# Performance work log

Measured on AMD Instinct MI355X. Metric: run time of the kernel, lower is better.

## Reference

```python
import jax, jax.numpy as jnp
import numpy as np

N_NODES = 100000
N_EDGES = 1600000
IN_DIM = 128
OUT_DIM = 128


def setup_inputs() -> dict:
    key = jax.random.key(0)
    k1, k2, k3, k4, k5 = jax.random.split(key, 5)
    h = jax.random.normal(k1, (N_NODES, IN_DIM), dtype=jnp.float32)
    # nn.Linear(in_dim, out_dim): W [out, in], b [out]
    W = jax.random.normal(k2, (OUT_DIM, IN_DIM), dtype=jnp.float32) * (1.0 / np.sqrt(IN_DIM))
    b = jax.random.normal(k3, (OUT_DIM,), dtype=jnp.float32) * 0.01
    edge_src = jax.random.randint(k4, (N_EDGES,), 0, N_NODES, dtype=jnp.int32)
    edge_dst = jax.random.randint(k5, (N_EDGES,), 0, N_NODES, dtype=jnp.int32)
    return {"h": h, "W": W, "b": b, "edge_src": edge_src, "edge_dst": edge_dst}


def reference(h, W, b, edge_src, edge_dst):
    n = h.shape[0]
    # in-degree of each node (edges point src -> dst), clamped to >= 1
    deg = jax.ops.segment_sum(jnp.ones_like(edge_dst, dtype=h.dtype), edge_dst, num_segments=n)
    norm = jnp.power(jnp.clip(deg, 1.0), -0.5)[:, None]  # [N, 1]
    hn = h * norm
    # copy_u + sum: gather source features, scatter-add to destinations (SpMM)
    agg = jax.ops.segment_sum(hn[edge_src], edge_dst, num_segments=n)  # [N, in_dim]
    out = (agg * norm) @ W.T + b
    return out
```

## Files before the change

kernel.cpp:

```cpp
#include <hip/hip_runtime.h>
#include <hip/hip_fp16.h>

#define DIM 128
#define TSH 8
#define TSZ 256
#define EBLK 4096

typedef _Float16 half8_t __attribute__((ext_vector_type(8)));
typedef float f32x4 __attribute__((ext_vector_type(4)));
typedef float f32x4v __attribute__((ext_vector_type(4)));


__global__ __launch_bounds__(1024) void hist_a(const int* __restrict__ dst,
                                               int* __restrict__ gh,
                                               int ne, int nblk, int nt,
                                               const float* __restrict__ W,
                                               _Float16* __restrict__ Wf) {
    __shared__ int h[512];
    int t = threadIdx.x;
    int blk = blockIdx.x;
    if (blk >= nblk) {
        int idx = (blk - nblk) * 1024 + t;
        int tile = idx >> 8;
        int kk = (idx >> 6) & 3;
        int lane = idx & 63;
        int nn = lane & 15, quad = lane >> 4;
        const float* wr = W + (tile * 16 + nn) * DIM + kk * 32 + quad * 8;
        _Float16* o = Wf + (size_t)idx * 8;
#pragma unroll
        for (int j = 0; j < 8; ++j) o[j] = (_Float16)wr[j];
        return;
    }
    if (t < 512) h[t] = 0;
    __syncthreads();
    int i0 = blk * EBLK + t;
#pragma unroll
    for (int u = 0; u < 4; ++u) {
        int i = i0 + u * 1024;
        if (i < ne) atomicAdd(&h[dst[i] >> TSH], 1);
    }
    __syncthreads();
    for (int k = t; k < nt; k += 1024) gh[k * nblk + blk] = h[k];
}

__global__ __launch_bounds__(256) void scan_a(int* __restrict__ g,
                                              int* __restrict__ bsum, int M) {
    __shared__ int wsum[4];
    int t = threadIdx.x;
    int base = blockIdx.x * 1024 + t * 4;
    int4 v;
    if (base + 3 < M) v = *(const int4*)(g + base);
    else {
        v.x = (base + 0 < M) ? g[base + 0] : 0;
        v.y = (base + 1 < M) ? g[base + 1] : 0;
        v.z = (base + 2 < M) ? g[base + 2] : 0;
        v.w = (base + 3 < M) ? g[base + 3] : 0;
    }
    int s3 = v.x + v.y + v.z + v.w;
    int lane = t & 63, wv = t >> 6;
    int x = s3;
#pragma unroll
    for (int off = 1; off < 64; off <<= 1) {
        int y = __shfl_up(x, off, 64);
        if (lane >= off) x += y;
    }
    if (lane == 63) wsum[wv] = x;
    __syncthreads();
    int woff = 0;
    for (int i = 0; i < wv; ++i) woff += wsum[i];
    int ex = woff + x - s3;
    int4 o;
    o.x = ex; o.y = ex + v.x; o.z = o.y + v.y; o.w = o.z + v.z;
    if (base + 3 < M) *(int4*)(g + base) = o;
    else {
        if (base + 0 < M) g[base + 0] = o.x;
        if (base + 1 < M) g[base + 1] = o.y;
        if (base + 2 < M) g[base + 2] = o.z;
        if (base + 3 < M) g[base + 3] = o.w;
    }
    if (t == 0) bsum[blockIdx.x] = wsum[0] + wsum[1] + wsum[2] + wsum[3];
}

__global__ __launch_bounds__(1024) void scatter_b(const int* __restrict__ src,
                                                  const int* __restrict__ dst,
                                                  const int* __restrict__ gh,
                                                  const int* __restrict__ bsum,
                                                  unsigned* __restrict__ tbuf,
                                                  int ne, int nblk, int M, int nt,
                                                  int nsc) {
    __shared__ int hD[512];
    __shared__ int ps[256];
    __shared__ int cur[512];
    __shared__ int gbl[256];
    __shared__ unsigned sval[EBLK];
    __shared__ unsigned short skey[EBLK];
    int t = threadIdx.x, blk = blockIdx.x;

    int bd = 0;
    if (t < 256) { bd = (t < nsc) ? bsum[t] : 0; ps[t] = bd; }
    __syncthreads();
    for (int off = 1; off < 256; off <<= 1) {
        int v = (t < 256 && t >= off) ? ps[t - off] : 0;
        __syncthreads();
        if (t < 256) ps[t] += v;
        __syncthreads();
    }
    if (t < 256) gbl[t] = ps[t] - bd;
    __syncthreads();

    int p0 = 0, c = 0;
    if (t < 512) {
        if (t < nt) {
            int idx = t * nblk + blk;
            p0 = gh[idx] + gbl[idx >> 10];
            int p1 = (idx + 1 < M) ? (gh[idx + 1] + gbl[(idx + 1) >> 10]) : ne;
            c = p1 - p0;
        }
        hD[t] = c;
    }
    __syncthreads();
    int h0 = 0, h1 = 0;
    if (t < 256) { h0 = hD[2 * t]; h1 = hD[2 * t + 1]; ps[t] = h0 + h1; }
    __syncthreads();
    for (int off = 1; off < 256; off <<= 1) {
        int v = (t < 256 && t >= off) ? ps[t - off] : 0;
        __syncthreads();
        if (t < 256) ps[t] += v;
        __syncthreads();
    }
    if (t < 256) {
        int ex0 = ps[t] - h0 - h1;
        cur[2 * t] = ex0;
        cur[2 * t + 1] = ex0 + h0;
    }
    __syncthreads();
    if (t < 512) hD[t] = p0 - cur[t];
    __syncthreads();

    int i0 = blk * EBLK + t;
#pragma unroll
    for (int u = 0; u < 4; ++u) {
        int i = i0 + u * 1024;
        if (i < ne) {
            int d = dst[i];
            int key = d >> TSH;
            int r = atomicAdd(&cur[key], 1);
            sval[r] = ((unsigned)src[i] << TSH) | (unsigned)(d & (TSZ - 1));
            skey[r] = (unsigned short)key;
        }
    }
    __syncthreads();
    int cnt = ne - blk * EBLK;
    if (cnt > EBLK) cnt = EBLK;
    for (int p = t; p < cnt; p += 1024)
        tbuf[hD[skey[p]] + p] = sval[p];
}

__global__ __launch_bounds__(1024) void tile_sort(const unsigned* __restrict__ tbuf,
                                                  const int* __restrict__ gh,
                                                  const int* __restrict__ bsum,
                                                  int* __restrict__ ebuf,
                                                  int* __restrict__ row_start,
                                                  const float* __restrict__ hsrc,
                                                  float2* __restrict__ hn,
                                                  int n, int ne, int nblk, int nt,
                                                  int nsc) {
    __shared__ int hist[TSZ];
    __shared__ int cur[TSZ];
    __shared__ int ps[256];
    __shared__ int gbl[256];
    __shared__ float scl[TSZ];
    int t = threadIdx.x;
    int tile = blockIdx.x;

    int bd = 0;
    if (t < 256) { bd = (t < nsc) ? bsum[t] : 0; ps[t] = bd; hist[t] = 0; }
    __syncthreads();
    for (int off = 1; off < 256; off <<= 1) {
        int v = (t < 256 && t >= off) ? ps[t - off] : 0;
        __syncthreads();
        if (t < 256) ps[t] += v;
        __syncthreads();
    }
    if (t < 256) gbl[t] = ps[t] - bd;
    __syncthreads();

    int i0 = tile * nblk;
    int ts = gh[i0] + gbl[i0 >> 10];
    int i1 = (tile + 1) * nblk;
    int te = (tile + 1 < nt) ? gh[i1] + gbl[i1 >> 10] : ne;

    for (int i = ts + t; i < te; i += 1024)
        atomicAdd(&hist[tbuf[i] & (TSZ - 1)], 1);
    __syncthreads();
    int d = 0;
    if (t < 256) { d = hist[t]; ps[t] = d; }
    __syncthreads();
    for (int off = 1; off < 256; off <<= 1) {
        int v = (t < 256 && t >= off) ? ps[t - off] : 0;
        __syncthreads();
        if (t < 256) ps[t] += v;
        __syncthreads();
    }
    if (t < 256) {
        int ex = ps[t] - d;
        cur[t] = ex;
        int node = tile * TSZ + t;
        if (node <= n) row_start[node] = ts + ex;
        scl[t] = rsqrtf((float)(d > 1 ? d : 1));
    }
    __syncthreads();
    for (int i = ts + t; i < te; i += 1024) {
        unsigned p = tbuf[i];
        int dl = (int)(p & (TSZ - 1));
        int r = atomicAdd(&cur[dl], 1);
        ebuf[ts + r] = (int)(p >> TSH);
    }
    int qbase = tile * 8192;
    for (int q = t; q < 8192; q += 1024) {
        int node = tile * TSZ + (q >> 5);
        if (node < n) {
            f32x4v v = __builtin_nontemporal_load((const f32x4v*)hsrc + qbase + q);
            float sc = scl[q >> 5];
            union { __half2 h2[2]; float2 f2; } u;
            u.h2[0] = __floats2half2_rn(v.x * sc, v.y * sc);
            u.h2[1] = __floats2half2_rn(v.z * sc, v.w * sc);
            hn[qbase + q] = u.f2;
        }
    }
}

__global__ __launch_bounds__(512) void gather_gemm(const float2* __restrict__ hn,
                                                   const int* __restrict__ ebuf,
                                                   const int* __restrict__ rs,
                                                   const _Float16* __restrict__ Wf,
                                                   const float* __restrict__ b,
                                                   float* __restrict__ out, int n) {
    __shared__ _Float16 xs[64 * 136];
    int tid = threadIdx.x;
    int g = tid >> 5, lane = tid & 31;

#pragma unroll
    for (int it = 0; it < 4; ++it) {
        int row = it * 16 + g;
        int node = blockIdx.x * 64 + row;
        union { __half2 h2[2]; float2 f2; } u;
        if (node < n) {
            int s0 = rs[node];
            int s1 = rs[node + 1];
            __half2 a0 = __floats2half2_rn(0.f, 0.f), a1 = a0;
            int i = s0;
            for (; i + 7 < s1; i += 8) {
                int e0 = ebuf[i], e1 = ebuf[i + 1], e2 = ebuf[i + 2], e3 = ebuf[i + 3];
                int e4 = ebuf[i + 4], e5 = ebuf[i + 5], e6 = ebuf[i + 6], e7 = ebuf[i + 7];
                float2 r0 = hn[(size_t)e0 * 32 + lane];
                float2 r1 = hn[(size_t)e1 * 32 + lane];
                float2 r2 = hn[(size_t)e2 * 32 + lane];
                float2 r3 = hn[(size_t)e3 * 32 + lane];
                float2 r4 = hn[(size_t)e4 * 32 + lane];
                float2 r5 = hn[(size_t)e5 * 32 + lane];
                float2 r6 = hn[(size_t)e6 * 32 + lane];
                float2 r7 = hn[(size_t)e7 * 32 + lane];
                const __half2* q0 = (const __half2*)&r0;
                const __half2* q1 = (const __half2*)&r1;
                const __half2* q2 = (const __half2*)&r2;
                const __half2* q3 = (const __half2*)&r3;
                const __half2* q4 = (const __half2*)&r4;
                const __half2* q5 = (const __half2*)&r5;
                const __half2* q6 = (const __half2*)&r6;
                const __half2* q7 = (const __half2*)&r7;
                a0 = __hadd2(a0, q0[0]); a1 = __hadd2(a1, q0[1]);
                a0 = __hadd2(a0, q1[0]); a1 = __hadd2(a1, q1[1]);
                a0 = __hadd2(a0, q2[0]); a1 = __hadd2(a1, q2[1]);
                a0 = __hadd2(a0, q3[0]); a1 = __hadd2(a1, q3[1]);
                a0 = __hadd2(a0, q4[0]); a1 = __hadd2(a1, q4[1]);
                a0 = __hadd2(a0, q5[0]); a1 = __hadd2(a1, q5[1]);
                a0 = __hadd2(a0, q6[0]); a1 = __hadd2(a1, q6[1]);
                a0 = __hadd2(a0, q7[0]); a1 = __hadd2(a1, q7[1]);
            }
            for (; i + 3 < s1; i += 4) {
                int e0 = ebuf[i], e1 = ebuf[i + 1], e2 = ebuf[i + 2], e3 = ebuf[i + 3];
                float2 r0 = hn[(size_t)e0 * 32 + lane];
                float2 r1 = hn[(size_t)e1 * 32 + lane];
                float2 r2 = hn[(size_t)e2 * 32 + lane];
                float2 r3 = hn[(size_t)e3 * 32 + lane];
                const __half2* q0 = (const __half2*)&r0;
                const __half2* q1 = (const __half2*)&r1;
                const __half2* q2 = (const __half2*)&r2;
                const __half2* q3 = (const __half2*)&r3;
                a0 = __hadd2(a0, q0[0]); a1 = __hadd2(a1, q0[1]);
                a0 = __hadd2(a0, q1[0]); a1 = __hadd2(a1, q1[1]);
                a0 = __hadd2(a0, q2[0]); a1 = __hadd2(a1, q2[1]);
                a0 = __hadd2(a0, q3[0]); a1 = __hadd2(a1, q3[1]);
            }
            for (; i < s1; ++i) {
                int e0 = ebuf[i];
                float2 r0 = hn[(size_t)e0 * 32 + lane];
                const __half2* q0 = (const __half2*)&r0;
                a0 = __hadd2(a0, q0[0]); a1 = __hadd2(a1, q0[1]);
            }
            int dn = s1 - s0;
            float nd = rsqrtf((float)(dn > 1 ? dn : 1));
            float2 f0 = __half22float2(a0), f1 = __half22float2(a1);
            u.h2[0] = __floats2half2_rn(f0.x * nd, f0.y * nd);
            u.h2[1] = __floats2half2_rn(f1.x * nd, f1.y * nd);
        } else {
            u.h2[0] = __floats2half2_rn(0.f, 0.f);
            u.h2[1] = u.h2[0];
        }
        *(float2*)(xs + row * 136 + lane * 4) = u.f2;
    }
    __syncthreads();

    int w = tid >> 6;
    int wl = tid & 63;
    int cn = wl & 15;
    int quad = wl >> 4;

    f32x4 acc[4] = {{0.f, 0.f, 0.f, 0.f}, {0.f, 0.f, 0.f, 0.f},
                    {0.f, 0.f, 0.f, 0.f}, {0.f, 0.f, 0.f, 0.f}};
#pragma unroll
    for (int kk = 0; kk < 4; ++kk) {
        half8_t bf = ((const half8_t*)Wf)[(w * 4 + kk) * 64 + wl];
#pragma unroll
        for (int rt = 0; rt < 4; ++rt) {
            half8_t af = *(const half8_t*)(xs + (rt * 16 + cn) * 136 + kk * 32 + quad * 8);
            acc[rt] = __builtin_amdgcn_mfma_f32_16x16x32_f16(af, bf, acc[rt], 0, 0, 0);
        }
    }
    float bj = b[w * 16 + cn];
    int node0 = blockIdx.x * 64;
#pragma unroll
    for (int rt = 0; rt < 4; ++rt) {
#pragma unroll
        for (int r = 0; r < 4; ++r) {
            int node = node0 + rt * 16 + quad * 4 + r;
            if (node < n)
                __builtin_nontemporal_store(acc[rt][r] + bj,
                                            &out[(size_t)node * DIM + w * 16 + cn]);
        }
    }
}

extern "C" void kernel_launch(void* const* d_in, const int* in_sizes, int n_in,
                              void* d_out, int out_size, void* d_ws, size_t ws_size,
                              hipStream_t stream) {
    const float* h = (const float*)d_in[0];
    const float* W = (const float*)d_in[1];
    const float* b = (const float*)d_in[2];
    const int* esrc = (const int*)d_in[3];
    const int* edst = (const int*)d_in[4];
    float* out = (float*)d_out;

    int n = in_sizes[0] / DIM;
    int ne = in_sizes[3];

    int nblk = (ne + EBLK - 1) / EBLK;
    int nt = (n + TSZ - 1) >> TSH;
    int M = nt * nblk;
    int nsc = (M + 1023) / 1024;

    float2* hn = (float2*)d_ws;
    _Float16* Wf = (_Float16*)(hn + (size_t)n * 32);
    int* row_start = (int*)(Wf + 16384);
    int* gh = row_start + (n + 1);
    int* gbsum = gh + M;
    unsigned* tbuf = (unsigned*)(gbsum + 256);
    int* ebuf = (int*)(tbuf + ne);

    hist_a<<<nblk + 2, 1024, 0, stream>>>(edst, gh, ne, nblk, nt, W, Wf);
    scan_a<<<nsc, 256, 0, stream>>>(gh, gbsum, M);
    scatter_b<<<nblk, 1024, 0, stream>>>(esrc, edst, gh, gbsum, tbuf, ne, nblk, M, nt, nsc);
    tile_sort<<<nt, 1024, 0, stream>>>(tbuf, gh, gbsum, ebuf, row_start, h, hn, n, ne, nblk, nt, nsc);
    gather_gemm<<<(n + 63) / 64, 512, 0, stream>>>(hn, ebuf, row_start, Wf, b, out, n);
}
```

Baseline: 216.4 us.

## Fuse per-tile edge sort with gather and GEMM, compute degrees via global atomics

Computes in-degree with global atomics in the histogram kernel and moves fp16 feature normalization into the scan kernel. The tile-sort kernel is merged with the gather+GEMM kernel, so each 256-node tile buckets its edges in LDS and aggregates and multiplies them directly. This removes the ebuf/row_start round trip and one launch. In exchange, the grid shrinks to about 391 large blocks with heavy LDS use, which lowers parallelism for the latency-bound gather. There is also a slow fallback path when a tile has more edges than fit in LDS.

```diff
diff --git a/kernel.cpp b/kernel.cpp
--- a/kernel.cpp
+++ b/kernel.cpp
@@ -5,27 +5,26 @@
 #define TSH 8
 #define TSZ 256
 #define EBLK 4096
+#define CAP 4608
 
 typedef _Float16 half8_t __attribute__((ext_vector_type(8)));
 typedef float f32x4 __attribute__((ext_vector_type(4)));
 typedef float f32x4v __attribute__((ext_vector_type(4)));
 
 
-__global__ __launch_bounds__(1024) void hist_a(const int* __restrict__ dst,
-                                               int* __restrict__ gh,
-                                               int ne, int nblk, int nt,
-                                               const float* __restrict__ W,
-                                               _Float16* __restrict__ Wf) {
+__global__ __launch_bounds__(1024) void k1_hist(const int* __restrict__ dst,
+                                                int* __restrict__ gh,
+                                                int* __restrict__ deg,
+                                                int ne, int neb, int nt,
+                                                const float* __restrict__ W,
+                                                _Float16* __restrict__ Wf) {
     __shared__ int h[512];
-    int t = threadIdx.x;
-    int blk = blockIdx.x;
-    if (blk >= nblk) {
-        int idx = (blk - nblk) * 1024 + t;
-        int tile = idx >> 8;
-        int kk = (idx >> 6) & 3;
-        int lane = idx & 63;
+    int t = threadIdx.x, blk = blockIdx.x;
+    if (blk >= neb) {
+        int idx = (blk - neb) * 1024 + t;
+        int ct = idx >> 8, kk = (idx >> 6) & 3, lane = idx & 63;
         int nn = lane & 15, quad = lane >> 4;
-        const float* wr = W + (tile * 16 + nn) * DIM + kk * 32 + quad * 8;
+        const float* wr = W + (ct * 16 + nn) * DIM + kk * 32 + quad * 8;
         _Float16* o = Wf + (size_t)idx * 8;
 #pragma unroll
         for (int j = 0; j < 8; ++j) o[j] = (_Float16)wr[j];
@@ -33,61 +32,69 @@
     }
     if (t < 512) h[t] = 0;
     __syncthreads();
-    int i0 = blk * EBLK + t;
-#pragma unroll
-    for (int u = 0; u < 4; ++u) {
-        int i = i0 + u * 1024;
-        if (i < ne) atomicAdd(&h[dst[i] >> TSH], 1);
-    }
-    __syncthreads();
-    for (int k = t; k < nt; k += 1024) gh[k * nblk + blk] = h[k];
-}
-
-__global__ __launch_bounds__(256) void scan_a(int* __restrict__ g,
-                                              int* __restrict__ bsum, int M) {
-    __shared__ int wsum[4];
-    int t = threadIdx.x;
-    int base = blockIdx.x * 1024 + t * 4;
-    int4 v;
-    if (base + 3 < M) v = *(const int4*)(g + base);
-    else {
-        v.x = (base + 0 < M) ? g[base + 0] : 0;
-        v.y = (base + 1 < M) ? g[base + 1] : 0;
-        v.z = (base + 2 < M) ? g[base + 2] : 0;
-        v.w = (base + 3 < M) ? g[base + 3] : 0;
-    }
-    int s3 = v.x + v.y + v.z + v.w;
-    int lane = t & 63, wv = t >> 6;
-    int x = s3;
-#pragma unroll
-    for (int off = 1; off < 64; off <<= 1) {
-        int y = __shfl_up(x, off, 64);
-        if (lane >= off) x += y;
-    }
-    if (lane == 63) wsum[wv] = x;
-    __syncthreads();
-    int woff = 0;
-    for (int i = 0; i < wv; ++i) woff += wsum[i];
-    int ex = woff + x - s3;
-    int4 o;
-    o.x = ex; o.y = ex + v.x; o.z = o.y + v.y; o.w = o.z + v.z;
-    if (base + 3 < M) *(int4*)(g + base) = o;
-    else {
-        if (base + 0 < M) g[base + 0] = o.x;
-        if (base + 1 < M) g[base + 1] = o.y;
-        if (base + 2 < M) g[base + 2] = o.z;
-        if (base + 3 < M) g[base + 3] = o.w;
-    }
-    if (t == 0) bsum[blockIdx.x] = wsum[0] + wsum[1] + wsum[2] + wsum[3];
-}
-
-__global__ __launch_bounds__(1024) void scatter_b(const int* __restrict__ src,
-                                                  const int* __restrict__ dst,
-                                                  const int* __restrict__ gh,
-                                                  const int* __restrict__ bsum,
-                                                  unsigned* __restrict__ tbuf,
-                                                  int ne, int nblk, int M, int nt,
-                                                  int nsc) {
+    int e0 = blk * EBLK;
+    int e1 = e0 + EBLK; if (e1 > ne) e1 = ne;
+    for (int i = e0 + t; i < e1; i += 1024) {
+        int d = dst[i];
+        atomicAdd(&h[d >> TSH], 1);
+        atomicAdd(&deg[d], 1);
+    }
+    __syncthreads();
+    for (int k = t; k < nt; k += 1024) gh[k * neb + blk] = h[k];
+}
+
+__global__ __launch_bounds__(1024) void k2_scan_hn(int* __restrict__ g,
+                                                   int* __restrict__ bsum,
+                                                   int M, int nsc,
+                                                   const int* __restrict__ deg,
+                                                   const float* __restrict__ hsrc,
+                                                   float2* __restrict__ hn,
+                                                   int n32) {
+    int t = threadIdx.x, blk = blockIdx.x;
+    if (blk < nsc) {
+        __shared__ int wsum[16];
+        int base = blk * 1024 + t;
+        int v = (base < M) ? g[base] : 0;
+        int lane = t & 63, wv = t >> 6;
+        int x = v;
+#pragma unroll
+        for (int off = 1; off < 64; off <<= 1) {
+            int y = __shfl_up(x, off, 64);
+            if (lane >= off) x += y;
+        }
+        if (lane == 63) wsum[wv] = x;
+        __syncthreads();
+        int woff = 0;
+        for (int i = 0; i < wv; ++i) woff += wsum[i];
+        if (base < M) g[base] = woff + x - v;
+        if (t == 0) {
+            int s = 0;
+#pragma unroll
+            for (int i = 0; i < 16; ++i) s += wsum[i];
+            bsum[blk] = s;
+        }
+        return;
+    }
+    int q = (blk - nsc) * 1024 + t;
+    if (q < n32) {
+        int node = q >> 5;
+        int dg = deg[node];
+        float sc = rsqrtf((float)(dg > 1 ? dg : 1));
+        f32x4v v = __builtin_nontemporal_load((const f32x4v*)hsrc + q);
+        union { __half2 h2[2]; float2 f2; } u;
+        u.h2[0] = __floats2half2_rn(v.x * sc, v.y * sc);
+        u.h2[1] = __floats2half2_rn(v.z * sc, v.w * sc);
+        hn[q] = u.f2;
+    }
+}
+
+__global__ __launch_bounds__(1024) void k3_scatter(const int* __restrict__ src,
+                                                   const int* __restrict__ dst,
+                                                   const int* __restrict__ gh,
+                                                   const int* __restrict__ bsum,
+                                                   unsigned* __restrict__ tbuf,
+                                                   int ne, int neb, int M, int nt,
+                                                   int nsc) {
     __shared__ int hD[512];
     __shared__ int ps[256];
     __shared__ int cur[512];
@@ -111,7 +118,7 @@
     int p0 = 0, c = 0;
     if (t < 512) {
         if (t < nt) {
-            int idx = t * nblk + blk;
+            int idx = t * neb + blk;
             p0 = gh[idx] + gbl[idx >> 10];
             int p1 = (idx + 1 < M) ? (gh[idx + 1] + gbl[(idx + 1) >> 10]) : ne;
             c = p1 - p0;
@@ -137,41 +144,36 @@
     if (t < 512) hD[t] = p0 - cur[t];
     __syncthreads();
 
-    int i0 = blk * EBLK + t;
-#pragma unroll
-    for (int u = 0; u < 4; ++u) {
-        int i = i0 + u * 1024;
-        if (i < ne) {
-            int d = dst[i];
-            int key = d >> TSH;
-            int r = atomicAdd(&cur[key], 1);
-            sval[r] = ((unsigned)src[i] << TSH) | (unsigned)(d & (TSZ - 1));
-            skey[r] = (unsigned short)key;
-        }
-    }
-    __syncthreads();
-    int cnt = ne - blk * EBLK;
-    if (cnt > EBLK) cnt = EBLK;
+    int e0 = blk * EBLK;
+    int e1 = e0 + EBLK; if (e1 > ne) e1 = ne;
+    for (int i = e0 + t; i < e1; i += 1024) {
+        int d = dst[i];
+        int key = d >> TSH;
+        int r = atomicAdd(&cur[key], 1);
+        sval[r] = ((unsigned)src[i] << TSH) | (unsigned)(d & (TSZ - 1));
+        skey[r] = (unsigned short)key;
+    }
+    __syncthreads();
+    int cnt = e1 - e0;
     for (int p = t; p < cnt; p += 1024)
         tbuf[hD[skey[p]] + p] = sval[p];
 }
 
-__global__ __launch_bounds__(1024) void tile_sort(const unsigned* __restrict__ tbuf,
-                                                  const int* __restrict__ gh,
-                                                  const int* __restrict__ bsum,
-                                                  int* __restrict__ ebuf,
-                                                  int* __restrict__ row_start,
-                                                  const float* __restrict__ hsrc,
-                                                  float2* __restrict__ hn,
-                                                  int n, int ne, int nblk, int nt,
-                                                  int nsc) {
+__global__ __launch_bounds__(1024) void k4_tile_gemm(
+        const unsigned* __restrict__ tbuf,
+        const int* __restrict__ gh, const int* __restrict__ bsum,
+        const float2* __restrict__ hn, const _Float16* __restrict__ Wf,
+        const float* __restrict__ b, float* __restrict__ out,
+        int n, int ne, int neb, int nt, int nsc, int M) {
+    __shared__ int gbl[256];
+    __shared__ int ps[256];
     __shared__ int hist[TSZ];
+    __shared__ int sst[TSZ];
     __shared__ int cur[TSZ];
-    __shared__ int ps[256];
-    __shared__ int gbl[256];
     __shared__ float scl[TSZ];
-    int t = threadIdx.x;
-    int tile = blockIdx.x;
+    __shared__ unsigned elB[CAP];
+    __shared__ _Float16 xs[128 * 136];
+    int t = threadIdx.x, tile = blockIdx.x;
 
     int bd = 0;
     if (t < 256) { bd = (t < nsc) ? bsum[t] : 0; ps[t] = bd; hist[t] = 0; }
@@ -185,10 +187,11 @@
     if (t < 256) gbl[t] = ps[t] - bd;
     __syncthreads();
 
-    int i0 = tile * nblk;
+    int i0 = tile * neb;
     int ts = gh[i0] + gbl[i0 >> 10];
-    int i1 = (tile + 1) * nblk;
+    int i1 = (tile + 1) * neb;
     int te = (tile + 1 < nt) ? gh[i1] + gbl[i1 >> 10] : ne;
+    int cnt = te - ts;
 
     for (int i = ts + t; i < te; i += 1024)
         atomicAdd(&hist[tbuf[i] & (TSZ - 1)], 1);
@@ -204,141 +207,97 @@
     }
     if (t < 256) {
         int ex = ps[t] - d;
+        sst[t] = ex;
         cur[t] = ex;
-        int node = tile * TSZ + t;
-        if (node <= n) row_start[node] = ts + ex;
         scl[t] = rsqrtf((float)(d > 1 ? d : 1));
     }
     __syncthreads();
-    for (int i = ts + t; i < te; i += 1024) {
-        unsigned p = tbuf[i];
-        int dl = (int)(p & (TSZ - 1));
-        int r = atomicAdd(&cur[dl], 1);
-        ebuf[ts + r] = (int)(p >> TSH);
-    }
-    int qbase = tile * 8192;
-    for (int q = t; q < 8192; q += 1024) {
-        int node = tile * TSZ + (q >> 5);
-        if (node < n) {
-            f32x4v v = __builtin_nontemporal_load((const f32x4v*)hsrc + qbase + q);
-            float sc = scl[q >> 5];
-            union { __half2 h2[2]; float2 f2; } u;
-            u.h2[0] = __floats2half2_rn(v.x * sc, v.y * sc);
-            u.h2[1] = __floats2half2_rn(v.z * sc, v.w * sc);
-            hn[qbase + q] = u.f2;
-        }
-    }
-}
-
-__global__ __launch_bounds__(512) void gather_gemm(const float2* __restrict__ hn,
-                                                   const int* __restrict__ ebuf,
-                                                   const int* __restrict__ rs,
-                                                   const _Float16* __restrict__ Wf,
-                                                   const float* __restrict__ b,
-                                                   float* __restrict__ out, int n) {
-    __shared__ _Float16 xs[64 * 136];
-    int tid = threadIdx.x;
-    int g = tid >> 5, lane = tid & 31;
-
-#pragma unroll
-    for (int it = 0; it < 4; ++it) {
-        int row = it * 16 + g;
-        int node = blockIdx.x * 64 + row;
-        union { __half2 h2[2]; float2 f2; } u;
-        if (node < n) {
-            int s0 = rs[node];
-            int s1 = rs[node + 1];
-            __half2 a0 = __floats2half2_rn(0.f, 0.f), a1 = a0;
-            int i = s0;
-            for (; i + 7 < s1; i += 8) {
-                int e0 = ebuf[i], e1 = ebuf[i + 1], e2 = ebuf[i + 2], e3 = ebuf[i + 3];
-                int e4 = ebuf[i + 4], e5 = ebuf[i + 5], e6 = ebuf[i + 6], e7 = ebuf[i + 7];
-                float2 r0 = hn[(size_t)e0 * 32 + lane];
-                float2 r1 = hn[(size_t)e1 * 32 + lane];
-                float2 r2 = hn[(size_t)e2 * 32 + lane];
-                float2 r3 = hn[(size_t)e3 * 32 + lane];
-                float2 r4 = hn[(size_t)e4 * 32 + lane];
-                float2 r5 = hn[(size_t)e5 * 32 + lane];
-                float2 r6 = hn[(size_t)e6 * 32 + lane];
-                float2 r7 = hn[(size_t)e7 * 32 + lane];
-                const __half2* q0 = (const __half2*)&r0;
-                const __half2* q1 = (const __half2*)&r1;
-                const __half2* q2 = (const __half2*)&r2;
-                const __half2* q3 = (const __half2*)&r3;
-                const __half2* q4 = (const __half2*)&r4;
-                const __half2* q5 = (const __half2*)&r5;
-                const __half2* q6 = (const __half2*)&r6;
-                const __half2* q7 = (const __half2*)&r7;
-                a0 = __hadd2(a0, q0[0]); a1 = __hadd2(a1, q0[1]);
-                a0 = __hadd2(a0, q1[0]); a1 = __hadd2(a1, q1[1]);
-                a0 = __hadd2(a0, q2[0]); a1 = __hadd2(a1, q2[1]);
-                a0 = __hadd2(a0, q3[0]); a1 = __hadd2(a1, q3[1]);
-                a0 = __hadd2(a0, q4[0]); a1 = __hadd2(a1, q4[1]);
-                a0 = __hadd2(a0, q5[0]); a1 = __hadd2(a1, q5[1]);
-                a0 = __hadd2(a0, q6[0]); a1 = __hadd2(a1, q6[1]);
-                a0 = __hadd2(a0, q7[0]); a1 = __hadd2(a1, q7[1]);
+
+    const _Float16* hp = (const _Float16*)hn;
+    int g = t >> 4, lane = t & 15;
+    int w = t >> 6, wl = t & 63, cn = wl & 15, quad = wl >> 4;
+    int ct = w & 7, rhg = w >> 3;
+
+    bool fast = (cnt <= CAP);
+    if (fast) {
+        for (int i = ts + t; i < te; i += 1024) {
+            unsigned p = tbuf[i];
+            int dl = (int)(p & (TSZ - 1));
+            int r = atomicAdd(&cur[dl], 1);
+            elB[r] = p >> TSH;
+        }
+        __syncthreads();
+    }
+
+    for (int hh = 0; hh < 2; ++hh) {
+#pragma unroll
+        for (int it = 0; it < 2; ++it) {
+            int dl = hh * 128 + it * 64 + g;
+            half8_t acc = {(_Float16)0, (_Float16)0, (_Float16)0, (_Float16)0,
+                           (_Float16)0, (_Float16)0, (_Float16)0, (_Float16)0};
+            if (fast) {
+                int s0 = sst[dl], c = hist[dl];
+                int j = s0, jend = s0 + c;
+                for (; j + 7 < jend; j += 8) {
+                    int e0 = elB[j], e1 = elB[j + 1], e2 = elB[j + 2], e3 = elB[j + 3];
+                    int e4 = elB[j + 4], e5 = elB[j + 5], e6 = elB[j + 6], e7 = elB[j + 7];
+                    half8_t r0 = *(const half8_t*)(hp + (size_t)e0 * 128 + lane * 8);
+                    half8_t r1 = *(const half8_t*)(hp + (size_t)e1 * 128 + lane * 8);
+                    half8_t r2 = *(const half8_t*)(hp + (size_t)e2 * 128 + lane * 8);
+                    half8_t r3 = *(const half8_t*)(hp + (size_t)e3 * 128 + lane * 8);
+                    half8_t r4 = *(const half8_t*)(hp + (size_t)e4 * 128 + lane * 8);
+                    half8_t r5 = *(const half8_t*)(hp + (size_t)e5 * 128 + lane * 8);
+                    half8_t r6 = *(const half8_t*)(hp + (size_t)e6 * 128 + lane * 8);
+                    half8_t r7 = *(const half8_t*)(hp + (size_t)e7 * 128 + lane * 8);
+                    acc += r0; acc += r1; acc += r2; acc += r3;
+                    acc += r4; acc += r5; acc += r6; acc += r7;
+                }
+                for (; j < jend; ++j) {
+                    int e0 = elB[j];
+                    acc += *(const half8_t*)(hp + (size_t)e0 * 128 + lane * 8);
+                }
+            } else {
+                for (int j = ts; j < te; ++j) {
+                    unsigned p = tbuf[j];
+                    if ((int)(p & (TSZ - 1)) == dl) {
+                        int e0 = (int)(p >> TSH);
+                        acc += *(const half8_t*)(hp + (size_t)e0 * 128 + lane * 8);
+                    }
+                }
             }
-            for (; i + 3 < s1; i += 4) {
-                int e0 = ebuf[i], e1 = ebuf[i + 1], e2 = ebuf[i + 2], e3 = ebuf[i + 3];
-                float2 r0 = hn[(size_t)e0 * 32 + lane];
-                float2 r1 = hn[(size_t)e1 * 32 + lane];
-                float2 r2 = hn[(size_t)e2 * 32 + lane];
-                float2 r3 = hn[(size_t)e3 * 32 + lane];
-                const __half2* q0 = (const __half2*)&r0;
-                const __half2* q1 = (const __half2*)&r1;
-                const __half2* q2 = (const __half2*)&r2;
-                const __half2* q3 = (const __half2*)&r3;
-                a0 = __hadd2(a0, q0[0]); a1 = __hadd2(a1, q0[1]);
-                a0 = __hadd2(a0, q1[0]); a1 = __hadd2(a1, q1[1]);
-                a0 = __hadd2(a0, q2[0]); a1 = __hadd2(a1, q2[1]);
-                a0 = __hadd2(a0, q3[0]); a1 = __hadd2(a1, q3[1]);
+            float nd = scl[dl];
+            half8_t o;
+#pragma unroll
+            for (int k2 = 0; k2 < 8; ++k2) o[k2] = (_Float16)((float)acc[k2] * nd);
+            *(half8_t*)(xs + (it * 64 + g) * 136 + lane * 8) = o;
+        }
+        __syncthreads();
+
+        f32x4 acc4[4] = {{0.f, 0.f, 0.f, 0.f}, {0.f, 0.f, 0.f, 0.f},
+                         {0.f, 0.f, 0.f, 0.f}, {0.f, 0.f, 0.f, 0.f}};
+#pragma unroll
+        for (int kk = 0; kk < 4; ++kk) {
+            half8_t bf = ((const half8_t*)Wf)[(ct * 4 + kk) * 64 + wl];
+#pragma unroll
+            for (int rt = 0; rt < 4; ++rt) {
+                half8_t af = *(const half8_t*)(xs + (rhg * 64 + rt * 16 + cn) * 136 +
+                                               kk * 32 + quad * 8);
+                acc4[rt] = __builtin_amdgcn_mfma_f32_16x16x32_f16(af, bf, acc4[rt], 0, 0, 0);
             }
-            for (; i < s1; ++i) {
-                int e0 = ebuf[i];
-                float2 r0 = hn[(size_t)e0 * 32 + lane];
-                const __half2* q0 = (const __half2*)&r0;
-                a0 = __hadd2(a0, q0[0]); a1 = __hadd2(a1, q0[1]);
+        }
+        float bj = b[ct * 16 + cn];
+        int node0 = tile * TSZ + hh * 128 + rhg * 64;
+#pragma unroll
+        for (int rt = 0; rt < 4; ++rt) {
+#pragma unroll
+            for (int r = 0; r < 4; ++r) {
+                int node = node0 + rt * 16 + quad * 4 + r;
+                if (node < n)
+                    __builtin_nontemporal_store(acc4[rt][r] + bj,
+                                                &out[(size_t)node * DIM + ct * 16 + cn]);
             }
-            int dn = s1 - s0;
-            float nd = rsqrtf((float)(dn > 1 ? dn : 1));
-            float2 f0 = __half22float2(a0), f1 = __half22float2(a1);
-            u.h2[0] = __floats2half2_rn(f0.x * nd, f0.y * nd);
-            u.h2[1] = __floats2half2_rn(f1.x * nd, f1.y * nd);
-        } else {
-            u.h2[0] = __floats2half2_rn(0.f, 0.f);
-            u.h2[1] = u.h2[0];
-        }
-        *(float2*)(xs + row * 136 + lane * 4) = u.f2;
-    }
-    __syncthreads();
-
-    int w = tid >> 6;
-    int wl = tid & 63;
-    int cn = wl & 15;
-    int quad = wl >> 4;
-
-    f32x4 acc[4] = {{0.f, 0.f, 0.f, 0.f}, {0.f, 0.f, 0.f, 0.f},
-                    {0.f, 0.f, 0.f, 0.f}, {0.f, 0.f, 0.f, 0.f}};
-#pragma unroll
-    for (int kk = 0; kk < 4; ++kk) {
-        half8_t bf = ((const half8_t*)Wf)[(w * 4 + kk) * 64 + wl];
-#pragma unroll
-        for (int rt = 0; rt < 4; ++rt) {
-            half8_t af = *(const half8_t*)(xs + (rt * 16 + cn) * 136 + kk * 32 + quad * 8);
-            acc[rt] = __builtin_amdgcn_mfma_f32_16x16x32_f16(af, bf, acc[rt], 0, 0, 0);
-        }
-    }
-    float bj = b[w * 16 + cn];
-    int node0 = blockIdx.x * 64;
-#pragma unroll
-    for (int rt = 0; rt < 4; ++rt) {
-#pragma unroll
-        for (int r = 0; r < 4; ++r) {
-            int node = node0 + rt * 16 + quad * 4 + r;
-            if (node < n)
-                __builtin_nontemporal_store(acc[rt][r] + bj,
-                                            &out[(size_t)node * DIM + w * 16 + cn]);
-        }
+        }
+        __syncthreads();
     }
 }
 
@@ -354,23 +313,25 @@
 
     int n = in_sizes[0] / DIM;
     int ne = in_sizes[3];
-
-    int nblk = (ne + EBLK - 1) / EBLK;
+    int n32 = n * 32;
+
+    int neb = (ne + EBLK - 1) / EBLK;
     int nt = (n + TSZ - 1) >> TSH;
-    int M = nt * nblk;
+    int M = nt * neb;
     int nsc = (M + 1023) / 1024;
 
     float2* hn = (float2*)d_ws;
     _Float16* Wf = (_Float16*)(hn + (size_t)n * 32);
-    int* row_start = (int*)(Wf + 16384);
-    int* gh = row_start + (n + 1);
-    int* gbsum = gh + M;
-    unsigned* tbuf = (unsigned*)(gbsum + 256);
-    int* ebuf = (int*)(tbuf + ne);
-
-    hist_a<<<nblk + 2, 1024, 0, stream>>>(edst, gh, ne, nblk, nt, W, Wf);
-    scan_a<<<nsc, 256, 0, stream>>>(gh, gbsum, M);
-    scatter_b<<<nblk, 1024, 0, stream>>>(esrc, edst, gh, gbsum, tbuf, ne, nblk, M, nt, nsc);
-    tile_sort<<<nt, 1024, 0, stream>>>(tbuf, gh, gbsum, ebuf, row_start, h, hn, n, ne, nblk, nt, nsc);
-    gather_gemm<<<(n + 63) / 64, 512, 0, stream>>>(hn, ebuf, row_start, Wf, b, out, n);
-}
+    int* deg = (int*)(Wf + 16384);
+    int* gh = deg + ((n + 3) & ~3);
+    int* bsum = gh + ((M + 3) & ~3);
+    unsigned* tbuf = (unsigned*)(bsum + 256);
+
+    hipMemsetAsync(deg, 0, (size_t)n * sizeof(int), stream);
+    k1_hist<<<neb + 2, 1024, 0, stream>>>(edst, gh, deg, ne, neb, nt, W, Wf);
+    k2_scan_hn<<<nsc + (n32 + 1023) / 1024, 1024, 0, stream>>>(gh, bsum, M, nsc,
+                                                               deg, h, hn, n32);
+    k3_scatter<<<neb, 1024, 0, stream>>>(esrc, edst, gh, bsum, tbuf, ne, neb, M, nt, nsc);
+    k4_tile_gemm<<<nt, 1024, 0, stream>>>(tbuf, gh, bsum, hn, Wf, b, out,
+                                          n, ne, neb, nt, nsc, M);
+}
```

Result: slower. 272.2 us (+25.8%).
